# Performance work log

Measured on AMD Instinct MI355X. Metric: run time of the kernel, lower is better.

The kernel has to match this reference:

```python
import jax, jax.numpy as jnp
import numpy as np

D_X, D_Y, HIDDEN, K = 256, 32, 256, 2
T = 50
SIG_MIN, SIG_MAX = 0.002, 1.0
N = 4096
D_XY = D_X + D_Y
D_IN = D_XY + 2 * HIDDEN  # 800


def setup_inputs() -> dict:
    key = jax.random.key(0)
    ks = jax.random.split(key, 12)
    def w(k, shape, fan):
        return (jax.random.normal(k, shape, jnp.float32) / np.sqrt(fan)).astype(jnp.float32)
    return {
        "xy0": jax.random.normal(ks[0], (N, D_XY), jnp.float32) * SIG_MAX,  # randn * sigma_max * extra_noise(=1)
        "t0": jax.random.randint(ks[1], (N,), 0, K),
        "t_embed": w(ks[2], (K, HIDDEN), 1),
        "tm_w1": w(ks[3], (1, HIDDEN), 1), "tm_b1": jnp.zeros((HIDDEN,), jnp.float32),
        "tm_w2": w(ks[4], (HIDDEN, HIDDEN), HIDDEN), "tm_b2": jnp.zeros((HIDDEN,), jnp.float32),
        "tr_w1": w(ks[5], (D_IN, HIDDEN), D_IN), "tr_b1": jnp.zeros((HIDDEN,), jnp.float32),
        "tr_w2": w(ks[6], (HIDDEN, HIDDEN), HIDDEN), "tr_b2": jnp.zeros((HIDDEN,), jnp.float32),
        "sh_w": w(ks[7], (HIDDEN, D_XY), HIDDEN), "sh_b": jnp.zeros((D_XY,), jnp.float32),
        "ch_w": w(ks[8], (HIDDEN, K), HIDDEN), "ch_b": jnp.zeros((K,), jnp.float32),
    }


def _sigma(t):
    return SIG_MIN * (SIG_MAX / SIG_MIN) ** t


def reference(xy0, t0, t_embed, tm_w1, tm_b1, tm_w2, tm_b2,
              tr_w1, tr_b1, tr_w2, tr_b2, sh_w, sh_b, ch_w, ch_b):
    n = xy0.shape[0]
    silu = jax.nn.silu
    base_key = jax.random.key(42)

    def net(xy, t, tau):
        te = t_embed[t]  # (n, H) embedding lookup
        # time_mlp on scalar tau -> (H,), broadcast over batch (tau is identical per row)
        tm = silu(tau * tm_w1[0] + tm_b1) @ tm_w2 + tm_b2
        tm = jnp.broadcast_to(tm, (n, HIDDEN))
        h = jnp.concatenate([xy, te, tm], axis=-1)  # (n, D_IN)
        h = silu(silu(h @ tr_w1 + tr_b1) @ tr_w2 + tr_b2)
        return h @ sh_w + sh_b, h @ ch_w + ch_b  # score (n, D_XY), logits (n, K)

    def body(carry, t_idx):
        xy, t = carry
        tau = t_idx.astype(jnp.float32) / T
        sig_t = _sigma(tau)
        sig_prev = _sigma((t_idx - 1).astype(jnp.float32) / T)
        step = sig_t ** 2 - sig_prev ** 2  # positive reverse-SDE step size
        score, logits = net(xy, t, tau)
        k1, k2 = jax.random.split(jax.random.fold_in(base_key, t_idx))
        xy = xy + step * score + jnp.sqrt(step) * jax.random.normal(k1, xy.shape, xy.dtype)
        t = jax.random.categorical(k2, logits, axis=-1)  # multinomial(softmax(logits), 1)
        return (xy, t), None

    steps = jnp.arange(T - 1, 0, -1)  # reversed(range(1, T))
    (xy, t), _ = jax.lax.scan(body, (xy0, t0), steps)
    return xy[:, :D_X], xy[:, D_X:], t
```

## Files before the change

kernel.cpp:

```cpp
#include <hip/hip_runtime.h>
#include <math.h>


#define DXY 288
#define HID 256
#define NTHR 512
#define OUT_Y_OFF 1048576
#define OUT_T_OFF 1179648
#define CT_FLOATS (50 * 512)
#define STEP_OFF  CT_FLOATS

typedef unsigned int u32;

__device__ __forceinline__ void tf2x32(u32 k0, u32 k1, u32 x0, u32 x1, u32& o0, u32& o1) {
  u32 ks2 = k0 ^ k1 ^ 0x1BD11BDAu;
#define TFR(r) { x0 += x1; x1 = (x1 << (r)) | (x1 >> (32 - (r))); x1 ^= x0; }
  x0 += k0; x1 += k1;
  TFR(13) TFR(15) TFR(26) TFR(6)
  x0 += k1;  x1 += ks2 + 1u;
  TFR(17) TFR(29) TFR(16) TFR(24)
  x0 += ks2; x1 += k0 + 2u;
  TFR(13) TFR(15) TFR(26) TFR(6)
  x0 += k0;  x1 += k1 + 3u;
  TFR(17) TFR(29) TFR(16) TFR(24)
  x0 += k1;  x1 += ks2 + 4u;
  TFR(13) TFR(15) TFR(26) TFR(6)
  x0 += ks2; x1 += k0 + 5u;
#undef TFR
  o0 = x0; o1 = x1;
}

__device__ __forceinline__ u32 pbits(u32 ka, u32 kb, u32 j) {
  u32 w0, w1;
  tf2x32(ka, kb, 0u, j, w0, w1);
  return w0 ^ w1;
}

__device__ __forceinline__ float u01f(u32 bits) {
  union { u32 i; float f; } v;
  v.i = (bits >> 9) | 0x3F800000u;
  return v.f - 1.0f;
}

__device__ __forceinline__ float erfinv32(float x) {
  float w = -log1pf(-x * x);
  float p;
  if (w < 5.0f) {
    w -= 2.5f;
    p = 2.81022636e-08f;
    p = fmaf(p, w, 3.43273939e-07f);
    p = fmaf(p, w, -3.5233877e-06f);
    p = fmaf(p, w, -4.39150654e-06f);
    p = fmaf(p, w, 0.00021858087f);
    p = fmaf(p, w, -0.00125372503f);
    p = fmaf(p, w, -0.00417768164f);
    p = fmaf(p, w, 0.246640727f);
    p = fmaf(p, w, 1.50140941f);
  } else {
    w = sqrtf(w) - 3.0f;
    p = -0.000200214257f;
    p = fmaf(p, w, 0.000100950558f);
    p = fmaf(p, w, 0.00134934322f);
    p = fmaf(p, w, -0.00367342844f);
    p = fmaf(p, w, 0.00573950773f);
    p = fmaf(p, w, -0.0076224613f);
    p = fmaf(p, w, 0.00943887047f);
    p = fmaf(p, w, 1.00167406f);
    p = fmaf(p, w, 2.83297682f);
  }
  return p * x;
}

__device__ __forceinline__ float nrmf(u32 bits) {
  float val = fmaf(u01f(bits), 2.0f, -0.99999994f);
  return 1.41421356f * erfinv32(val);
}
__device__ __forceinline__ float gumf(u32 bits) {
  float u = fmaxf(u01f(bits), 1.17549435e-38f);
  return -logf(-logf(u));
}
__device__ __forceinline__ float siluf(float x) {
  return x / (1.0f + expf(-x));
}
__device__ __forceinline__ void fma4(float a, const float4& b, float* acc) {
  acc[0] = fmaf(a, b.x, acc[0]);
  acc[1] = fmaf(a, b.y, acc[1]);
  acc[2] = fmaf(a, b.z, acc[2]);
  acc[3] = fmaf(a, b.w, acc[3]);
}

__global__ void precompute_ct(
    const float* __restrict__ t_embed,
    const float* __restrict__ tm_w1, const float* __restrict__ tm_b1,
    const float* __restrict__ tm_w2, const float* __restrict__ tm_b2,
    const float* __restrict__ tr_w1, const float* __restrict__ tr_b1,
    float* __restrict__ ws)
{
  const int t = blockIdx.x + 1;
  const int c = threadIdx.x;
  __shared__ float tmpre[HID];
  __shared__ float tmv[HID];
  const float tau = (float)t / 50.0f;

  tmpre[c] = siluf(fmaf(tau, tm_w1[c], tm_b1[c]));
  __syncthreads();
  {
    float acc = tm_b2[c];
    for (int i = 0; i < HID; i++)
      acc = fmaf(tmpre[i], tm_w2[i * HID + c], acc);
    tmv[c] = acc;
  }
  __syncthreads();
  float D = 0.f;
  for (int i = 0; i < HID; i++)
    D = fmaf(tmv[i], tr_w1[(544 + i) * HID + c], D);
  float ce0 = tr_b1[c], ce1 = tr_b1[c];
  for (int i = 0; i < HID; i++) {
    ce0 = fmaf(t_embed[i], tr_w1[(288 + i) * HID + c], ce0);
    ce1 = fmaf(t_embed[HID + i], tr_w1[(288 + i) * HID + c], ce1);
  }
  ws[t * 512 + c] = ce0 + D;
  ws[t * 512 + 256 + c] = ce1 + D;

  if (c == 0) {
    const double lt = 6.214608098422191;
    float sig_t = (float)(0.002 * exp(((double)t / 50.0) * lt));
    float sig_p = (float)(0.002 * exp(((double)(t - 1) / 50.0) * lt));
    float stepf = sig_t * sig_t - sig_p * sig_p;
    ws[STEP_OFF + 2 * t] = stepf;
    ws[STEP_OFF + 2 * t + 1] = sqrtf(stepf);
  }
}

__global__ __launch_bounds__(NTHR, 2) void sampler_k(
    const float* __restrict__ xy0, const int* __restrict__ t0,
    const float* __restrict__ tr_w1,
    const float* __restrict__ tr_w2, const float* __restrict__ tr_b2,
    const float* __restrict__ sh_w, const float* __restrict__ sh_b,
    const float* __restrict__ ch_w, const float* __restrict__ ch_b,
    const float* __restrict__ ws,
    float* __restrict__ out)
{
  __shared__ float xy_s[16][DXY];
  __shared__ float h_s[16][HID];

  const int tid = threadIdx.x;
  const int lane = tid & 63;
  const int w = tid >> 6;
  const int rA = w, rB = w + 8;
  const int row0 = blockIdx.x * 16;
  const int gA = row0 + rA, gB = row0 + rB;
  const int c0 = lane * 4;
  const bool xl = (lane < 8);
  const int cX = 256 + lane * 4;

  {
    const float4* sA = (const float4*)(xy0 + gA * DXY);
    const float4* sB = (const float4*)(xy0 + gB * DXY);
    *(float4*)&xy_s[rA][c0] = sA[lane];
    *(float4*)&xy_s[rB][c0] = sB[lane];
    if (xl) {
      *(float4*)&xy_s[rA][cX] = sA[64 + lane];
      *(float4*)&xy_s[rB][cX] = sB[64 + lane];
    }
  }
  int tcA = t0[gA];
  int tcB = t0[gB];

  float chw0[4], chw1[4];
  #pragma unroll
  for (int j = 0; j < 4; j++) {
    chw0[j] = ch_w[(c0 + j) * 2 + 0];
    chw1[j] = ch_w[(c0 + j) * 2 + 1];
  }
  const float4 b2r = *(const float4*)(tr_b2 + c0);
  const float cb0 = ch_b[0], cb1 = ch_b[1];
  const float4 sbm = *(const float4*)(sh_b + c0);
  const int cEx = 256 + (lane & 31);
  const int rEx = (lane < 32) ? rA : rB;
  const u32 gEx = (u32)(row0 + rEx);
  const float sbEx = sh_b[cEx];

  #pragma unroll 1
  for (int t_idx = 49; t_idx >= 1; --t_idx) {
    const float stepf = ws[STEP_OFF + 2 * t_idx];
    const float sstep = ws[STEP_OFF + 2 * t_idx + 1];

    u32 f0, f1, k1a, k1b, k2a, k2b;
    tf2x32(0u, 42u, 0u, (u32)t_idx, f0, f1);
    tf2x32(f0, f1, 0u, 0u, k1a, k1b);
    tf2x32(f0, f1, 0u, 1u, k2a, k2b);

    const float* ct = ws + t_idx * 512;
    const float4 ctA = *(const float4*)(ct + tcA * 256 + c0);
    const float4 ctB = *(const float4*)(ct + tcB * 256 + c0);

    {
      float aA[4] = {0.f, 0.f, 0.f, 0.f};
      float aB[4] = {0.f, 0.f, 0.f, 0.f};
      const float* wp = tr_w1 + c0;
      #pragma unroll 4
      for (int i = 0; i < DXY; i += 4) {
        float4 xA = *(const float4*)&xy_s[rA][i];
        float4 xB = *(const float4*)&xy_s[rB][i];
        float4 b0 = *(const float4*)(wp + (i + 0) * HID);
        float4 b1 = *(const float4*)(wp + (i + 1) * HID);
        float4 b2 = *(const float4*)(wp + (i + 2) * HID);
        float4 b3 = *(const float4*)(wp + (i + 3) * HID);
        fma4(xA.x, b0, aA); fma4(xA.y, b1, aA); fma4(xA.z, b2, aA); fma4(xA.w, b3, aA);
        fma4(xB.x, b0, aB); fma4(xB.y, b1, aB); fma4(xB.z, b2, aB); fma4(xB.w, b3, aB);
      }
      float4 oA, oB;
      oA.x = siluf(aA[0] + ctA.x); oA.y = siluf(aA[1] + ctA.y);
      oA.z = siluf(aA[2] + ctA.z); oA.w = siluf(aA[3] + ctA.w);
      oB.x = siluf(aB[0] + ctB.x); oB.y = siluf(aB[1] + ctB.y);
      oB.z = siluf(aB[2] + ctB.z); oB.w = siluf(aB[3] + ctB.w);
      *(float4*)&h_s[rA][c0] = oA;
      *(float4*)&h_s[rB][c0] = oB;
    }

    {
      float aA[4] = {0.f, 0.f, 0.f, 0.f};
      float aB[4] = {0.f, 0.f, 0.f, 0.f};
      const float* wp = tr_w2 + c0;
      #pragma unroll 4
      for (int i = 0; i < HID; i += 4) {
        float4 hA = *(const float4*)&h_s[rA][i];
        float4 hB = *(const float4*)&h_s[rB][i];
        float4 b0 = *(const float4*)(wp + (i + 0) * HID);
        float4 b1 = *(const float4*)(wp + (i + 1) * HID);
        float4 b2 = *(const float4*)(wp + (i + 2) * HID);
        float4 b3 = *(const float4*)(wp + (i + 3) * HID);
        fma4(hA.x, b0, aA); fma4(hA.y, b1, aA); fma4(hA.z, b2, aA); fma4(hA.w, b3, aA);
        fma4(hB.x, b0, aB); fma4(hB.y, b1, aB); fma4(hB.z, b2, aB); fma4(hB.w, b3, aB);
      }
      float4 hA2, hB2;
      hA2.x = siluf(aA[0] + b2r.x); hA2.y = siluf(aA[1] + b2r.y);
      hA2.z = siluf(aA[2] + b2r.z); hA2.w = siluf(aA[3] + b2r.w);
      hB2.x = siluf(aB[0] + b2r.x); hB2.y = siluf(aB[1] + b2r.y);
      hB2.z = siluf(aB[2] + b2r.z); hB2.w = siluf(aB[3] + b2r.w);
      *(float4*)&h_s[rA][c0] = hA2;
      *(float4*)&h_s[rB][c0] = hB2;

      float pA0 = hA2.x * chw0[0] + hA2.y * chw0[1] + hA2.z * chw0[2] + hA2.w * chw0[3];
      float pA1 = hA2.x * chw1[0] + hA2.y * chw1[1] + hA2.z * chw1[2] + hA2.w * chw1[3];
      float pB0 = hB2.x * chw0[0] + hB2.y * chw0[1] + hB2.z * chw0[2] + hB2.w * chw0[3];
      float pB1 = hB2.x * chw1[0] + hB2.y * chw1[1] + hB2.z * chw1[2] + hB2.w * chw1[3];
      #pragma unroll
      for (int off = 32; off > 0; off >>= 1) {
        pA0 += __shfl_xor(pA0, off);
        pA1 += __shfl_xor(pA1, off);
        pB0 += __shfl_xor(pB0, off);
        pB1 += __shfl_xor(pB1, off);
      }
      u32 grow = (lane & 2) ? (u32)gB : (u32)gA;
      float g = gumf(pbits(k2a, k2b, grow * 2u + (u32)(lane & 1)));
      float g0 = __shfl(g, 0), g1 = __shfl(g, 1);
      float g2 = __shfl(g, 2), g3 = __shfl(g, 3);
      tcA = (pA1 + cb1 + g1 > pA0 + cb0 + g0) ? 1 : 0;
      tcB = (pB1 + cb1 + g3 > pB0 + cb0 + g2) ? 1 : 0;
    }

    {
      float sA[4] = {0.f, 0.f, 0.f, 0.f};
      float sB[4] = {0.f, 0.f, 0.f, 0.f};
      #pragma unroll 4
      for (int i = 0; i < HID; i += 4) {
        float4 hA = *(const float4*)&h_s[rA][i];
        float4 hB = *(const float4*)&h_s[rB][i];
        const float* bp = sh_w + i * DXY + c0;
        float4 b0 = *(const float4*)(bp);
        float4 b1 = *(const float4*)(bp + DXY);
        float4 b2 = *(const float4*)(bp + 2 * DXY);
        float4 b3 = *(const float4*)(bp + 3 * DXY);
        fma4(hA.x, b0, sA); fma4(hA.y, b1, sA); fma4(hA.z, b2, sA); fma4(hA.w, b3, sA);
        fma4(hB.x, b0, sB); fma4(hB.y, b1, sB); fma4(hB.z, b2, sB); fma4(hB.w, b3, sB);
      }
      const u32 jA = (u32)gA * 288u + (u32)c0;
      const u32 jB = (u32)gB * 288u + (u32)c0;
      float4 xA = *(const float4*)&xy_s[rA][c0];
      float4 xB = *(const float4*)&xy_s[rB][c0];
      xA.x = fmaf(sstep, nrmf(pbits(k1a, k1b, jA + 0u)), fmaf(stepf, sA[0] + sbm.x, xA.x));
      xA.y = fmaf(sstep, nrmf(pbits(k1a, k1b, jA + 1u)), fmaf(stepf, sA[1] + sbm.y, xA.y));
      xA.z = fmaf(sstep, nrmf(pbits(k1a, k1b, jA + 2u)), fmaf(stepf, sA[2] + sbm.z, xA.z));
      xA.w = fmaf(sstep, nrmf(pbits(k1a, k1b, jA + 3u)), fmaf(stepf, sA[3] + sbm.w, xA.w));
      xB.x = fmaf(sstep, nrmf(pbits(k1a, k1b, jB + 0u)), fmaf(stepf, sB[0] + sbm.x, xB.x));
      xB.y = fmaf(sstep, nrmf(pbits(k1a, k1b, jB + 1u)), fmaf(stepf, sB[1] + sbm.y, xB.y));
      xB.z = fmaf(sstep, nrmf(pbits(k1a, k1b, jB + 2u)), fmaf(stepf, sB[2] + sbm.z, xB.z));
      xB.w = fmaf(sstep, nrmf(pbits(k1a, k1b, jB + 3u)), fmaf(stepf, sB[3] + sbm.w, xB.w));
      *(float4*)&xy_s[rA][c0] = xA;
      *(float4*)&xy_s[rB][c0] = xB;
    }

    {
      float sE = 0.f;
      #pragma unroll 4
      for (int i = 0; i < HID; i += 4) {
        float4 hE = *(const float4*)&h_s[rEx][i];
        const float* bp = sh_w + i * DXY + cEx;
        sE = fmaf(hE.x, bp[0],
             fmaf(hE.y, bp[DXY],
             fmaf(hE.z, bp[2 * DXY],
             fmaf(hE.w, bp[3 * DXY], sE))));
      }
      u32 jE = gEx * 288u + (u32)cEx;
      float nE = nrmf(pbits(k1a, k1b, jE));
      xy_s[rEx][cEx] = fmaf(sstep, nE, fmaf(stepf, sE + sbEx, xy_s[rEx][cEx]));
    }
  }

  {
    float4 vA = *(const float4*)&xy_s[rA][c0];
    float4 vB = *(const float4*)&xy_s[rB][c0];
    *(float4*)(out + gA * 256 + c0) = vA;
    *(float4*)(out + gB * 256 + c0) = vB;
    if (xl) {
      float4 yA = *(const float4*)&xy_s[rA][cX];
      float4 yB = *(const float4*)&xy_s[rB][cX];
      *(float4*)(out + OUT_Y_OFF + gA * 32 + lane * 4) = yA;
      *(float4*)(out + OUT_Y_OFF + gB * 32 + lane * 4) = yB;
    }
    if (lane == 0) {
      out[OUT_T_OFF + gA] = (float)tcA;
      out[OUT_T_OFF + gB] = (float)tcB;
    }
  }
}

extern "C" void kernel_launch(void* const* d_in, const int* in_sizes, int n_in,
                              void* d_out, int out_size, void* d_ws, size_t ws_size,
                              hipStream_t stream) {
  (void)in_sizes; (void)n_in; (void)ws_size; (void)out_size;
  const float* xy0     = (const float*)d_in[0];
  const int*   t0      = (const int*)d_in[1];
  const float* t_embed = (const float*)d_in[2];
  const float* tm_w1   = (const float*)d_in[3];
  const float* tm_b1   = (const float*)d_in[4];
  const float* tm_w2   = (const float*)d_in[5];
  const float* tm_b2   = (const float*)d_in[6];
  const float* tr_w1   = (const float*)d_in[7];
  const float* tr_b1   = (const float*)d_in[8];
  const float* tr_w2   = (const float*)d_in[9];
  const float* tr_b2   = (const float*)d_in[10];
  const float* sh_w    = (const float*)d_in[11];
  const float* sh_b    = (const float*)d_in[12];
  const float* ch_w    = (const float*)d_in[13];
  const float* ch_b    = (const float*)d_in[14];
  float* ws  = (float*)d_ws;
  float* out = (float*)d_out;

  precompute_ct<<<49, 256, 0, stream>>>(t_embed, tm_w1, tm_b1, tm_w2, tm_b2,
                                        tr_w1, tr_b1, ws);
  sampler_k<<<256, NTHR, 0, stream>>>(xy0, t0, tr_w1, tr_w2, tr_b2,
                                      sh_w, sh_b, ch_w, ch_b, ws, out);
}
```

Baseline: 2.721 ms.

## Remap threads so each warp covers a column slice across 16 rows

Previously each warp owned two rows and every lane read full weight rows, so each of the eight warps streamed the whole weight matrices from global/L2. Now each warp owns a 32-column slice and handles two rows per lane group, so each weight element is read by one warp only. This requires block-wide __syncthreads between layers, separate h1/h2 shared buffers with padding, and a shared-memory tcur/ct table that is reloaded each step. The extra barriers and the cross-warp reduction for the logits add synchronization cost.

```diff
diff --git a/kernel.cpp b/kernel.cpp
--- a/kernel.cpp
+++ b/kernel.cpp
@@ -5,6 +5,8 @@
 #define DXY 288
 #define HID 256
 #define NTHR 512
+#define XYP 292
+#define HP  260
 #define OUT_Y_OFF 1048576
 #define OUT_T_OFF 1179648
 #define CT_FLOATS (50 * 512)
@@ -141,45 +143,42 @@
     const float* __restrict__ ws,
     float* __restrict__ out)
 {
-  __shared__ float xy_s[16][DXY];
-  __shared__ float h_s[16][HID];
+  __shared__ float xy_s[16][XYP];
+  __shared__ float h1_s[16][HP];
+  __shared__ float h2_s[16][HP];
+  __shared__ float ct_s[2][HID];
+  __shared__ int tcur_s[16];
 
   const int tid = threadIdx.x;
   const int lane = tid & 63;
   const int w = tid >> 6;
-  const int rA = w, rB = w + 8;
-  const int row0 = blockIdx.x * 16;
-  const int gA = row0 + rA, gB = row0 + rB;
-  const int c0 = lane * 4;
-  const bool xl = (lane < 8);
-  const int cX = 256 + lane * 4;
-
-  {
-    const float4* sA = (const float4*)(xy0 + gA * DXY);
-    const float4* sB = (const float4*)(xy0 + gB * DXY);
-    *(float4*)&xy_s[rA][c0] = sA[lane];
-    *(float4*)&xy_s[rB][c0] = sB[lane];
-    if (xl) {
-      *(float4*)&xy_s[rA][cX] = sA[64 + lane];
-      *(float4*)&xy_s[rB][cX] = sB[64 + lane];
-    }
-  }
-  int tcA = t0[gA];
-  int tcB = t0[gB];
+  const int row0g = blockIdx.x * 16;
+
+  const int r0 = lane >> 3;
+  const int r1 = r0 + 8;
+  const int cg = w * 32 + (lane & 7) * 4;
+  const int rE = lane >> 2;
+  const int cE = 256 + w * 4 + (lane & 3);
+
+  for (int idx = tid; idx < 16 * (DXY / 4); idx += NTHR) {
+    int r = idx / (DXY / 4);
+    int q = idx - r * (DXY / 4);
+    *(float4*)&xy_s[r][q * 4] = *(const float4*)(xy0 + (row0g + r) * DXY + q * 4);
+  }
+  if (tid < 16) tcur_s[tid] = t0[row0g + tid];
+  ((float*)ct_s)[tid] = ws[49 * 512 + tid];
 
   float chw0[4], chw1[4];
   #pragma unroll
   for (int j = 0; j < 4; j++) {
-    chw0[j] = ch_w[(c0 + j) * 2 + 0];
-    chw1[j] = ch_w[(c0 + j) * 2 + 1];
-  }
-  const float4 b2r = *(const float4*)(tr_b2 + c0);
+    chw0[j] = ch_w[(lane * 4 + j) * 2 + 0];
+    chw1[j] = ch_w[(lane * 4 + j) * 2 + 1];
+  }
+  const float4 b2r = *(const float4*)(tr_b2 + cg);
   const float cb0 = ch_b[0], cb1 = ch_b[1];
-  const float4 sbm = *(const float4*)(sh_b + c0);
-  const int cEx = 256 + (lane & 31);
-  const int rEx = (lane < 32) ? rA : rB;
-  const u32 gEx = (u32)(row0 + rEx);
-  const float sbEx = sh_b[cEx];
+  const float4 sbm = *(const float4*)(sh_b + cg);
+  const float sbE = sh_b[cE];
+  __syncthreads();
 
   #pragma unroll 1
   for (int t_idx = 49; t_idx >= 1; --t_idx) {
@@ -191,18 +190,15 @@
     tf2x32(f0, f1, 0u, 0u, k1a, k1b);
     tf2x32(f0, f1, 0u, 1u, k2a, k2b);
 
-    const float* ct = ws + t_idx * 512;
-    const float4 ctA = *(const float4*)(ct + tcA * 256 + c0);
-    const float4 ctB = *(const float4*)(ct + tcB * 256 + c0);
-
-    {
+    {
+      const int tc0 = tcur_s[r0], tc1 = tcur_s[r1];
       float aA[4] = {0.f, 0.f, 0.f, 0.f};
       float aB[4] = {0.f, 0.f, 0.f, 0.f};
-      const float* wp = tr_w1 + c0;
+      const float* wp = tr_w1 + cg;
       #pragma unroll 4
       for (int i = 0; i < DXY; i += 4) {
-        float4 xA = *(const float4*)&xy_s[rA][i];
-        float4 xB = *(const float4*)&xy_s[rB][i];
+        float4 xA = *(const float4*)&xy_s[r0][i];
+        float4 xB = *(const float4*)&xy_s[r1][i];
         float4 b0 = *(const float4*)(wp + (i + 0) * HID);
         float4 b1 = *(const float4*)(wp + (i + 1) * HID);
         float4 b2 = *(const float4*)(wp + (i + 2) * HID);
@@ -210,23 +206,26 @@
         fma4(xA.x, b0, aA); fma4(xA.y, b1, aA); fma4(xA.z, b2, aA); fma4(xA.w, b3, aA);
         fma4(xB.x, b0, aB); fma4(xB.y, b1, aB); fma4(xB.z, b2, aB); fma4(xB.w, b3, aB);
       }
+      const float4 ctA = *(const float4*)&ct_s[tc0][cg];
+      const float4 ctB = *(const float4*)&ct_s[tc1][cg];
       float4 oA, oB;
       oA.x = siluf(aA[0] + ctA.x); oA.y = siluf(aA[1] + ctA.y);
       oA.z = siluf(aA[2] + ctA.z); oA.w = siluf(aA[3] + ctA.w);
       oB.x = siluf(aB[0] + ctB.x); oB.y = siluf(aB[1] + ctB.y);
       oB.z = siluf(aB[2] + ctB.z); oB.w = siluf(aB[3] + ctB.w);
-      *(float4*)&h_s[rA][c0] = oA;
-      *(float4*)&h_s[rB][c0] = oB;
-    }
+      *(float4*)&h1_s[r0][cg] = oA;
+      *(float4*)&h1_s[r1][cg] = oB;
+    }
+    __syncthreads();
 
     {
       float aA[4] = {0.f, 0.f, 0.f, 0.f};
       float aB[4] = {0.f, 0.f, 0.f, 0.f};
-      const float* wp = tr_w2 + c0;
+      const float* wp = tr_w2 + cg;
       #pragma unroll 4
       for (int i = 0; i < HID; i += 4) {
-        float4 hA = *(const float4*)&h_s[rA][i];
-        float4 hB = *(const float4*)&h_s[rB][i];
+        float4 hA = *(const float4*)&h1_s[r0][i];
+        float4 hB = *(const float4*)&h1_s[r1][i];
         float4 b0 = *(const float4*)(wp + (i + 0) * HID);
         float4 b1 = *(const float4*)(wp + (i + 1) * HID);
         float4 b2 = *(const float4*)(wp + (i + 2) * HID);
@@ -234,18 +233,23 @@
         fma4(hA.x, b0, aA); fma4(hA.y, b1, aA); fma4(hA.z, b2, aA); fma4(hA.w, b3, aA);
         fma4(hB.x, b0, aB); fma4(hB.y, b1, aB); fma4(hB.z, b2, aB); fma4(hB.w, b3, aB);
       }
-      float4 hA2, hB2;
-      hA2.x = siluf(aA[0] + b2r.x); hA2.y = siluf(aA[1] + b2r.y);
-      hA2.z = siluf(aA[2] + b2r.z); hA2.w = siluf(aA[3] + b2r.w);
-      hB2.x = siluf(aB[0] + b2r.x); hB2.y = siluf(aB[1] + b2r.y);
-      hB2.z = siluf(aB[2] + b2r.z); hB2.w = siluf(aB[3] + b2r.w);
-      *(float4*)&h_s[rA][c0] = hA2;
-      *(float4*)&h_s[rB][c0] = hB2;
-
-      float pA0 = hA2.x * chw0[0] + hA2.y * chw0[1] + hA2.z * chw0[2] + hA2.w * chw0[3];
-      float pA1 = hA2.x * chw1[0] + hA2.y * chw1[1] + hA2.z * chw1[2] + hA2.w * chw1[3];
-      float pB0 = hB2.x * chw0[0] + hB2.y * chw0[1] + hB2.z * chw0[2] + hB2.w * chw0[3];
-      float pB1 = hB2.x * chw1[0] + hB2.y * chw1[1] + hB2.z * chw1[2] + hB2.w * chw1[3];
+      float4 oA, oB;
+      oA.x = siluf(aA[0] + b2r.x); oA.y = siluf(aA[1] + b2r.y);
+      oA.z = siluf(aA[2] + b2r.z); oA.w = siluf(aA[3] + b2r.w);
+      oB.x = siluf(aB[0] + b2r.x); oB.y = siluf(aB[1] + b2r.y);
+      oB.z = siluf(aB[2] + b2r.z); oB.w = siluf(aB[3] + b2r.w);
+      *(float4*)&h2_s[r0][cg] = oA;
+      *(float4*)&h2_s[r1][cg] = oB;
+    }
+    __syncthreads();
+
+    {
+      float4 hL0 = *(const float4*)&h2_s[2 * w][lane * 4];
+      float4 hL1 = *(const float4*)&h2_s[2 * w + 1][lane * 4];
+      float pA0 = hL0.x * chw0[0] + hL0.y * chw0[1] + hL0.z * chw0[2] + hL0.w * chw0[3];
+      float pA1 = hL0.x * chw1[0] + hL0.y * chw1[1] + hL0.z * chw1[2] + hL0.w * chw1[3];
+      float pB0 = hL1.x * chw0[0] + hL1.y * chw0[1] + hL1.z * chw0[2] + hL1.w * chw0[3];
+      float pB1 = hL1.x * chw1[0] + hL1.y * chw1[1] + hL1.z * chw1[2] + hL1.w * chw1[3];
       #pragma unroll
       for (int off = 32; off > 0; off >>= 1) {
         pA0 += __shfl_xor(pA0, off);
@@ -253,33 +257,35 @@
         pB0 += __shfl_xor(pB0, off);
         pB1 += __shfl_xor(pB1, off);
       }
-      u32 grow = (lane & 2) ? (u32)gB : (u32)gA;
+      u32 grow = (u32)(row0g + 2 * w + ((lane >> 1) & 1));
       float g = gumf(pbits(k2a, k2b, grow * 2u + (u32)(lane & 1)));
       float g0 = __shfl(g, 0), g1 = __shfl(g, 1);
       float g2 = __shfl(g, 2), g3 = __shfl(g, 3);
-      tcA = (pA1 + cb1 + g1 > pA0 + cb0 + g0) ? 1 : 0;
-      tcB = (pB1 + cb1 + g3 > pB0 + cb0 + g2) ? 1 : 0;
+      if (lane == 0) {
+        tcur_s[2 * w]     = (pA1 + cb1 + g1 > pA0 + cb0 + g0) ? 1 : 0;
+        tcur_s[2 * w + 1] = (pB1 + cb1 + g3 > pB0 + cb0 + g2) ? 1 : 0;
+      }
     }
 
     {
       float sA[4] = {0.f, 0.f, 0.f, 0.f};
       float sB[4] = {0.f, 0.f, 0.f, 0.f};
+      const float* wp = sh_w + cg;
       #pragma unroll 4
       for (int i = 0; i < HID; i += 4) {
-        float4 hA = *(const float4*)&h_s[rA][i];
-        float4 hB = *(const float4*)&h_s[rB][i];
-        const float* bp = sh_w + i * DXY + c0;
-        float4 b0 = *(const float4*)(bp);
-        float4 b1 = *(const float4*)(bp + DXY);
-        float4 b2 = *(const float4*)(bp + 2 * DXY);
-        float4 b3 = *(const float4*)(bp + 3 * DXY);
+        float4 hA = *(const float4*)&h2_s[r0][i];
+        float4 hB = *(const float4*)&h2_s[r1][i];
+        float4 b0 = *(const float4*)(wp + (i + 0) * DXY);
+        float4 b1 = *(const float4*)(wp + (i + 1) * DXY);
+        float4 b2 = *(const float4*)(wp + (i + 2) * DXY);
+        float4 b3 = *(const float4*)(wp + (i + 3) * DXY);
         fma4(hA.x, b0, sA); fma4(hA.y, b1, sA); fma4(hA.z, b2, sA); fma4(hA.w, b3, sA);
         fma4(hB.x, b0, sB); fma4(hB.y, b1, sB); fma4(hB.z, b2, sB); fma4(hB.w, b3, sB);
       }
-      const u32 jA = (u32)gA * 288u + (u32)c0;
-      const u32 jB = (u32)gB * 288u + (u32)c0;
-      float4 xA = *(const float4*)&xy_s[rA][c0];
-      float4 xB = *(const float4*)&xy_s[rB][c0];
+      const u32 jA = (u32)(row0g + r0) * 288u + (u32)cg;
+      const u32 jB = (u32)(row0g + r1) * 288u + (u32)cg;
+      float4 xA = *(const float4*)&xy_s[r0][cg];
+      float4 xB = *(const float4*)&xy_s[r1][cg];
       xA.x = fmaf(sstep, nrmf(pbits(k1a, k1b, jA + 0u)), fmaf(stepf, sA[0] + sbm.x, xA.x));
       xA.y = fmaf(sstep, nrmf(pbits(k1a, k1b, jA + 1u)), fmaf(stepf, sA[1] + sbm.y, xA.y));
       xA.z = fmaf(sstep, nrmf(pbits(k1a, k1b, jA + 2u)), fmaf(stepf, sA[2] + sbm.z, xA.z));
@@ -288,43 +294,42 @@
       xB.y = fmaf(sstep, nrmf(pbits(k1a, k1b, jB + 1u)), fmaf(stepf, sB[1] + sbm.y, xB.y));
       xB.z = fmaf(sstep, nrmf(pbits(k1a, k1b, jB + 2u)), fmaf(stepf, sB[2] + sbm.z, xB.z));
       xB.w = fmaf(sstep, nrmf(pbits(k1a, k1b, jB + 3u)), fmaf(stepf, sB[3] + sbm.w, xB.w));
-      *(float4*)&xy_s[rA][c0] = xA;
-      *(float4*)&xy_s[rB][c0] = xB;
+      *(float4*)&xy_s[r0][cg] = xA;
+      *(float4*)&xy_s[r1][cg] = xB;
     }
 
     {
       float sE = 0.f;
+      const float* wp = sh_w + cE;
       #pragma unroll 4
       for (int i = 0; i < HID; i += 4) {
-        float4 hE = *(const float4*)&h_s[rEx][i];
-        const float* bp = sh_w + i * DXY + cEx;
+        float4 hE = *(const float4*)&h2_s[rE][i];
+        const float* bp = wp + i * DXY;
         sE = fmaf(hE.x, bp[0],
              fmaf(hE.y, bp[DXY],
              fmaf(hE.z, bp[2 * DXY],
              fmaf(hE.w, bp[3 * DXY], sE))));
       }
-      u32 jE = gEx * 288u + (u32)cEx;
+      u32 jE = (u32)(row0g + rE) * 288u + (u32)cE;
       float nE = nrmf(pbits(k1a, k1b, jE));
-      xy_s[rEx][cEx] = fmaf(sstep, nE, fmaf(stepf, sE + sbEx, xy_s[rEx][cEx]));
-    }
-  }
-
-  {
-    float4 vA = *(const float4*)&xy_s[rA][c0];
-    float4 vB = *(const float4*)&xy_s[rB][c0];
-    *(float4*)(out + gA * 256 + c0) = vA;
-    *(float4*)(out + gB * 256 + c0) = vB;
-    if (xl) {
-      float4 yA = *(const float4*)&xy_s[rA][cX];
-      float4 yB = *(const float4*)&xy_s[rB][cX];
-      *(float4*)(out + OUT_Y_OFF + gA * 32 + lane * 4) = yA;
-      *(float4*)(out + OUT_Y_OFF + gB * 32 + lane * 4) = yB;
-    }
-    if (lane == 0) {
-      out[OUT_T_OFF + gA] = (float)tcA;
-      out[OUT_T_OFF + gB] = (float)tcB;
-    }
-  }
+      xy_s[rE][cE] = fmaf(sstep, nE, fmaf(stepf, sE + sbE, xy_s[rE][cE]));
+    }
+
+    if (t_idx > 1) ((float*)ct_s)[tid] = ws[(t_idx - 1) * 512 + tid];
+    __syncthreads();
+  }
+
+  for (int idx = tid; idx < 16 * 64; idx += NTHR) {
+    int r = idx >> 6;
+    int c4 = (idx & 63) * 4;
+    *(float4*)(out + (row0g + r) * 256 + c4) = *(const float4*)&xy_s[r][c4];
+  }
+  for (int idx = tid; idx < 16 * 8; idx += NTHR) {
+    int r = idx >> 3;
+    int c4 = (idx & 7) * 4;
+    *(float4*)(out + OUT_Y_OFF + (row0g + r) * 32 + c4) = *(const float4*)&xy_s[r][256 + c4];
+  }
+  if (tid < 16) out[OUT_T_OFF + row0g + tid] = (float)tcur_s[tid];
 }
 
 extern "C" void kernel_launch(void* const* d_in, const int* in_sizes, int n_in,
```

Measured after the change: 2.758 ms. No clear change (+1.3%).
